# Optimization experiments

Hardware: AMD Instinct MI355X
Metric: run time of the kernel (lower is better)

## Reference

```python
import jax, jax.numpy as jnp
import numpy as np

KERNEL_SIZES = (3, 5, 7)
NUM_HEAD = 6
DIM = 192
K_SCALES = 3
HEADS_PER_SCALE = NUM_HEAD // K_SCALES  # 2
HEAD_DIM = DIM // NUM_HEAD              # 32
SCALE = HEAD_DIM ** -0.5


def _nbr_idx(L, K):
    # NATTEN non-causal, dilation=1: window centered on query, clamped at edges.
    start = jnp.clip(jnp.arange(L) - K // 2, 0, L - K)
    return start[:, None] + jnp.arange(K)  # [L, K]


def _na3d_branch(xi, K):
    # xi: [B, D, H, W, C] with C = 3 * HEADS_PER_SCALE * HEAD_DIM
    B, D, H, W, C = xi.shape
    qkv = xi.reshape(B, D, H, W, 3, HEADS_PER_SCALE, HEAD_DIM).transpose(4, 0, 5, 1, 2, 3, 6)
    q, k, v = qkv[0] * SCALE, qkv[1], qkv[2]  # each [B, h, D, H, W, hd]

    idd, idh, idw = _nbr_idx(D, K), _nbr_idx(H, K), _nbr_idx(W, K)

    def gather(t):
        t = jnp.take(t, idd, axis=2)  # [B,h,D,K,H,W,hd]
        t = jnp.take(t, idh, axis=4)  # [B,h,D,K,H,K,W,hd]
        t = jnp.take(t, idw, axis=6)  # [B,h,D,K,H,K,W,K,hd]
        return t

    kn = gather(k)
    vn = gather(v)
    # attention logits over the K^3 neighborhood per query
    attn = jnp.einsum('bndhwc,bndihjwkc->bndhwijk', q, kn)
    attn = jax.nn.softmax(attn.reshape(B, HEADS_PER_SCALE, D, H, W, K ** 3), axis=-1)
    attn = attn.reshape(B, HEADS_PER_SCALE, D, H, W, K, K, K)
    y = jnp.einsum('bndhwijk,bndihjwkc->bndhwc', attn, vn)
    # [B,h,D,H,W,hd] -> [B,D,H,W,h*hd]
    return y.transpose(0, 2, 3, 4, 1, 5).reshape(B, D, H, W, HEADS_PER_SCALE * HEAD_DIM)


def setup_inputs() -> dict:
    key = jax.random.key(0)
    k0, k1, k2 = jax.random.split(key, 3)
    x = jax.random.normal(k0, (1, 8, 24, 24, DIM), dtype=jnp.float32)
    W_qkv = jax.random.normal(k1, (DIM, 3 * DIM), dtype=jnp.float32) * 0.02
    b_qkv = jnp.zeros((3 * DIM,), dtype=jnp.float32)
    W_proj = jax.random.normal(k2, (DIM, DIM), dtype=jnp.float32) * 0.02
    b_proj = jnp.zeros((DIM,), dtype=jnp.float32)
    return {'x': x, 'W_qkv': W_qkv, 'b_qkv': b_qkv, 'W_proj': W_proj, 'b_proj': b_proj}


def reference(x, W_qkv, b_qkv, W_proj, b_proj):
    qkv = x @ W_qkv + b_qkv  # [B,D,H,W,3*DIM]
    # torch.split with channels [DIM, DIM, DIM]
    chunks = jnp.split(qkv, K_SCALES, axis=4)
    ys = [_na3d_branch(chunks[i], KERNEL_SIZES[i]) for i in range(K_SCALES)]
    y = jnp.concatenate(ys, axis=4)  # [B,D,H,W,DIM]
    return y @ W_proj + b_proj
```

## Files before the change

kernel.cpp:

```cpp
#include <hip/hip_runtime.h>

typedef unsigned short ushort_t;
typedef unsigned int uint_t;
typedef __attribute__((ext_vector_type(8))) short short8;
typedef __attribute__((ext_vector_type(4))) float f32x4;

constexpr int DD = 8, HH = 24, WW = 24;
constexpr int NQ = DD * HH * WW;
constexpr int CIN = 192;
constexpr int CQKV = 576;
constexpr int KP = 576;
constexpr float ATT_SCALE = 0.17677669529663687f;
constexpr int NROW = DD * HH;

__device__ __forceinline__ ushort_t bf16h(float x) {
    uint_t u = __float_as_uint(x);
    u += 0x7FFFu + ((u >> 16) & 1u);
    return (ushort_t)(u >> 16);
}
__device__ __forceinline__ float bf16f(ushort_t h) {
    return __uint_as_float(((uint_t)h) << 16);
}
__device__ __forceinline__ float2 unpack2(uint_t u) {
    return make_float2(__uint_as_float(u << 16),
                       __uint_as_float(u & 0xffff0000u));
}

constexpr int EB0 = 0;
constexpr int EB1 = NROW * 2 * WW * 2;
constexpr int EB2 = EB1 + NROW * 3 * WW * 2;
constexpr int ETOT = EB2 + NROW * 4 * WW * 2;

__global__ __launch_bounds__(256)
void convert_w_kernel(const float* __restrict__ Wq, const float* __restrict__ Wp,
                      ushort_t* __restrict__ Bq, ushort_t* __restrict__ Bp)
{
    __shared__ float T[32][36];
    int b = blockIdx.x;
    const float* W; ushort_t* Bb; int N;
    int kt, nt;
    if (b < 108) { W = Wq; Bb = Bq; N = CQKV; kt = b % 6; nt = b / 6; }
    else         { b -= 108; W = Wp; Bb = Bp; N = CIN; kt = b % 6; nt = b / 6; }
    const int k0 = kt * 32, n0 = nt * 32;
    const int tid = threadIdx.x;

    #pragma unroll
    for (int p = 0; p < 4; ++p) {
        int e = p * 256 + tid;
        int r = e >> 5, c = e & 31;
        T[c][r] = W[(long)(k0 + r) * N + n0 + c];
    }
    __syncthreads();
    const int n = tid >> 3;
    const int k4 = (tid & 7) * 4;
    float4 v = *(const float4*)(&T[n][k4]);
    ushort4 hv, lv;
    hv.x = bf16h(v.x); lv.x = bf16h(v.x - bf16f(hv.x));
    hv.y = bf16h(v.y); lv.y = bf16h(v.y - bf16f(hv.y));
    hv.z = bf16h(v.z); lv.z = bf16h(v.z - bf16f(hv.z));
    hv.w = bf16h(v.w); lv.w = bf16h(v.w - bf16f(hv.w));
    const int k = k0 + k4;
    const int g = k >> 6;
    const int kc = k & 63;
    ushort_t* row = Bb + (long)(n0 + n) * KP + g * 192 + kc;
    *(ushort4*)(row)       = hv;
    *(ushort4*)(row + 64)  = lv;
    *(ushort4*)(row + 128) = hv;
}

__global__ __launch_bounds__(256)
void gemm_mfma_kernel(const float* __restrict__ A, const ushort_t* __restrict__ Bb,
                      const float* __restrict__ bias, ushort_t* __restrict__ Cout, int N)
{
    __shared__ ushort_t As[64][72];
    __shared__ ushort_t Bs[64][72];
    __shared__ float Ct[64][68];

    const int tid = threadIdx.x;
    const int bm = blockIdx.x * 64;
    const int bn = blockIdx.y * 64;

    const int wv = tid >> 6;
    const int lane = tid & 63;
    const int lm = lane & 15;
    const int quad = lane >> 4;
    const int wr = (wv >> 1) * 32;
    const int wc = (wv & 1) * 32;

    const int ar = tid >> 4;
    const int ac4 = (tid & 15) * 4;
    const int br0 = tid >> 3;
    const int bc0 = (tid & 7) * 8;

    f32x4 acc[2][2] = {};

    #pragma unroll
    for (int g = 0; g < 3; ++g) {
        float4 av[4];
        ushort4 hv4[4];
        #pragma unroll
        for (int p = 0; p < 4; ++p)
            av[p] = *(const float4*)(A + (long)(bm + ar + p * 16) * CIN + g * 64 + ac4);

        #pragma unroll
        for (int ph = 0; ph < 3; ++ph) {
            const int kk = g * 192 + ph * 64;
            uint4 b0 = *(const uint4*)(Bb + (long)(bn + br0) * KP + kk + bc0);
            uint4 b1 = *(const uint4*)(Bb + (long)(bn + br0 + 32) * KP + kk + bc0);
            __syncthreads();
            if (ph == 0) {
                #pragma unroll
                for (int p = 0; p < 4; ++p) {
                    float4 v = av[p];
                    ushort4 hv;
                    hv.x = bf16h(v.x); hv.y = bf16h(v.y);
                    hv.z = bf16h(v.z); hv.w = bf16h(v.w);
                    hv4[p] = hv;
                    *(ushort4*)(&As[ar + p * 16][ac4]) = hv;
                }
            } else if (ph == 2) {
                #pragma unroll
                for (int p = 0; p < 4; ++p) {
                    float4 v = av[p];
                    ushort4 lv;
                    lv.x = bf16h(v.x - bf16f(hv4[p].x));
                    lv.y = bf16h(v.y - bf16f(hv4[p].y));
                    lv.z = bf16h(v.z - bf16f(hv4[p].z));
                    lv.w = bf16h(v.w - bf16f(hv4[p].w));
                    *(ushort4*)(&As[ar + p * 16][ac4]) = lv;
                }
            }
            *(uint4*)(&Bs[br0][bc0]) = b0;
            *(uint4*)(&Bs[br0 + 32][bc0]) = b1;
            __syncthreads();

            #pragma unroll
            for (int ks = 0; ks < 64; ks += 32) {
                short8 af0 = *(const short8*)(&As[wr + lm][ks + quad * 8]);
                short8 af1 = *(const short8*)(&As[wr + 16 + lm][ks + quad * 8]);
                short8 bf0 = *(const short8*)(&Bs[wc + lm][ks + quad * 8]);
                short8 bf1 = *(const short8*)(&Bs[wc + 16 + lm][ks + quad * 8]);
                acc[0][0] = __builtin_amdgcn_mfma_f32_16x16x32_bf16(af0, bf0, acc[0][0], 0, 0, 0);
                acc[0][1] = __builtin_amdgcn_mfma_f32_16x16x32_bf16(af0, bf1, acc[0][1], 0, 0, 0);
                acc[1][0] = __builtin_amdgcn_mfma_f32_16x16x32_bf16(af1, bf0, acc[1][0], 0, 0, 0);
                acc[1][1] = __builtin_amdgcn_mfma_f32_16x16x32_bf16(af1, bf1, acc[1][1], 0, 0, 0);
            }
        }
    }

    #pragma unroll
    for (int tc = 0; tc < 2; ++tc) {
        const float bv = bias[bn + wc + tc * 16 + lm];
        #pragma unroll
        for (int tr = 0; tr < 2; ++tr) {
            #pragma unroll
            for (int reg = 0; reg < 4; ++reg)
                Ct[wr + tr * 16 + quad * 4 + reg][wc + tc * 16 + lm] = acc[tr][tc][reg] + bv;
        }
    }
    __syncthreads();
    const int orow = tid >> 4;
    const int oc4 = (tid & 15) * 4;
    #pragma unroll
    for (int p = 0; p < 4; ++p) {
        const int r = orow + p * 16;
        float4 v = *(const float4*)(&Ct[r][oc4]);
        ushort4 hv;
        hv.x = bf16h(v.x); hv.y = bf16h(v.y); hv.z = bf16h(v.z); hv.w = bf16h(v.w);
        *(ushort4*)(Cout + (long)(bm + r) * N + bn + oc4) = hv;
    }
}

__global__ __launch_bounds__(256)
void gemm_proj_kernel(const float* __restrict__ accs, const float* __restrict__ stats,
                      const ushort_t* __restrict__ Bb, const float* __restrict__ bias,
                      float* __restrict__ Cout)
{
    __shared__ ushort_t As[64][72];
    __shared__ ushort_t Bs[64][72];
    __shared__ float Ct[64][68];

    const int tid = threadIdx.x;
    const int bm = blockIdx.x * 64;
    const int bn = blockIdx.y * 64;

    const int wv = tid >> 6;
    const int lane = tid & 63;
    const int lm = lane & 15;
    const int quad = lane >> 4;
    const int wr = (wv >> 1) * 32;
    const int wc = (wv & 1) * 32;

    const int ar = tid >> 4;
    const int ac4 = (tid & 15) * 4;
    const int a_hd = ac4 >> 5;
    const int a_cc = ac4 & 31;
    const int br0 = tid >> 3;
    const int bc0 = (tid & 7) * 8;

    f32x4 acc[2][2] = {};

    #pragma unroll
    for (int g = 0; g < 3; ++g) {
        const int CK = g + 2;
        const int eb = (g == 0) ? EB0 : (g == 1 ? EB1 : EB2);

        float4 av[4];
        ushort4 hv4[4];
        #pragma unroll
        for (int p = 0; p < 4; ++p) {
            const int q = bm + ar + p * 16;
            const int rr = q / WW;
            const int w = q - rr * WW;
            const int e0 = eb + (rr * CK) * (WW * 2) + w * 2 + a_hd;
            float S = 0.f;
            float4 a = make_float4(0.f, 0.f, 0.f, 0.f);
            #pragma unroll
            for (int c = 0; c < 4; ++c) {
                if (c < CK) {
                    const int e = e0 + c * (WW * 2);
                    S += stats[e];
                    const float4 t = *(const float4*)(accs + (long)e * 32 + a_cc);
                    a.x += t.x; a.y += t.y; a.z += t.z; a.w += t.w;
                }
            }
            const float rs = 1.0f / S;
            av[p] = make_float4(a.x * rs, a.y * rs, a.z * rs, a.w * rs);
        }

        #pragma unroll
        for (int ph = 0; ph < 3; ++ph) {
            const int kk = g * 192 + ph * 64;
            uint4 b0 = *(const uint4*)(Bb + (long)(bn + br0) * KP + kk + bc0);
            uint4 b1 = *(const uint4*)(Bb + (long)(bn + br0 + 32) * KP + kk + bc0);
            __syncthreads();
            if (ph == 0) {
                #pragma unroll
                for (int p = 0; p < 4; ++p) {
                    float4 v = av[p];
                    ushort4 hv;
                    hv.x = bf16h(v.x); hv.y = bf16h(v.y);
                    hv.z = bf16h(v.z); hv.w = bf16h(v.w);
                    hv4[p] = hv;
                    *(ushort4*)(&As[ar + p * 16][ac4]) = hv;
                }
            } else if (ph == 2) {
                #pragma unroll
                for (int p = 0; p < 4; ++p) {
                    float4 v = av[p];
                    ushort4 lv;
                    lv.x = bf16h(v.x - bf16f(hv4[p].x));
                    lv.y = bf16h(v.y - bf16f(hv4[p].y));
                    lv.z = bf16h(v.z - bf16f(hv4[p].z));
                    lv.w = bf16h(v.w - bf16f(hv4[p].w));
                    *(ushort4*)(&As[ar + p * 16][ac4]) = lv;
                }
            }
            *(uint4*)(&Bs[br0][bc0]) = b0;
            *(uint4*)(&Bs[br0 + 32][bc0]) = b1;
            __syncthreads();

            #pragma unroll
            for (int ks = 0; ks < 64; ks += 32) {
                short8 af0 = *(const short8*)(&As[wr + lm][ks + quad * 8]);
                short8 af1 = *(const short8*)(&As[wr + 16 + lm][ks + quad * 8]);
                short8 bf0 = *(const short8*)(&Bs[wc + lm][ks + quad * 8]);
                short8 bf1 = *(const short8*)(&Bs[wc + 16 + lm][ks + quad * 8]);
                acc[0][0] = __builtin_amdgcn_mfma_f32_16x16x32_bf16(af0, bf0, acc[0][0], 0, 0, 0);
                acc[0][1] = __builtin_amdgcn_mfma_f32_16x16x32_bf16(af0, bf1, acc[0][1], 0, 0, 0);
                acc[1][0] = __builtin_amdgcn_mfma_f32_16x16x32_bf16(af1, bf0, acc[1][0], 0, 0, 0);
                acc[1][1] = __builtin_amdgcn_mfma_f32_16x16x32_bf16(af1, bf1, acc[1][1], 0, 0, 0);
            }
        }
    }

    #pragma unroll
    for (int tc = 0; tc < 2; ++tc) {
        const float bv = bias[bn + wc + tc * 16 + lm];
        #pragma unroll
        for (int tr = 0; tr < 2; ++tr) {
            #pragma unroll
            for (int reg = 0; reg < 4; ++reg)
                Ct[wr + tr * 16 + quad * 4 + reg][wc + tc * 16 + lm] = acc[tr][tc][reg] + bv;
        }
    }
    __syncthreads();
    const int orow = tid >> 4;
    const int oc4 = (tid & 15) * 4;
    #pragma unroll
    for (int p = 0; p < 4; ++p) {
        const int r = orow + p * 16;
        float4 v = *(const float4*)(&Ct[r][oc4]);
        *(float4*)(Cout + (long)(bm + r) * CIN + bn + oc4) = v;
    }
}

constexpr int KROW = 72;
constexpr int RBUF = WW * KROW;

template<int K>
__device__ __forceinline__
void split_chunk(const ushort_t* __restrict__ qkv,
                 float* __restrict__ accs, float* __restrict__ stats,
                 int r, int c, int nchunks, int scale, int ebase,
                 int w, int hd, int d8, int tid,
                 ushort_t* __restrict__ ksh, ushort_t* __restrict__ vsh)
{
    const int i0 = 2 * c;
    const int ni = (K - i0) < 2 ? (K - i0) : 2;
    const int NT = ni * K;

    const int dq = r / HH, hq = r % HH;
    int sd = dq - K / 2; sd = sd < 0 ? 0 : (sd > DD - K ? DD - K : sd);
    int sh = hq - K / 2; sh = sh < 0 ? 0 : (sh > HH - K ? HH - K : sh);
    int sw = w  - K / 2; sw = sw < 0 ? 0 : (sw > WW - K ? WW - K : sw);

    const int q = (dq * HH + hq) * WW + w;

    uint4 qu = *(const uint4*)(qkv + (long)q * CQKV + scale * 192 + hd * 32 + d8 * 8);
    float2 qf[4] = {unpack2(qu.x), unpack2(qu.y), unpack2(qu.z), unpack2(qu.w)};
    #pragma unroll
    for (int t = 0; t < 4; ++t) {
        qf[t].x *= ATT_SCALE;
        qf[t].y *= ATT_SCALE;
    }

    const int lw = tid >> 3;
    const int c8 = (tid & 7) * 8;

    auto load_kv = [&](int buf, int t) {
        int i = i0 + t / K;
        int j = t - (t / K) * K;
        const ushort_t* p = qkv + (long)(((sd + i) * HH + (sh + j)) * WW + lw) * CQKV
                          + scale * 192 + c8;
        uint4 kk = *(const uint4*)(p + 64);
        uint4 vv = *(const uint4*)(p + 128);
        *(uint4*)(ksh + buf * RBUF + lw * KROW + c8) = kk;
        *(uint4*)(vsh + buf * RBUF + lw * KROW + c8) = vv;
    };

    float sum = 0.f;
    float2 acc[4] = {};
    const int choff = hd * 32 + d8 * 8;

    load_kv(0, 0);
    if (NT > 1) load_kv(1, 1);

    for (int t = 0; t < NT; ++t) {
        __syncthreads();
        if (t + 2 < NT) load_kv((t + 2) % 3, t + 2);

        const ushort_t* kb = ksh + (t % 3) * RBUF + choff;
        const ushort_t* vb = vsh + (t % 3) * RBUF + choff;
        #pragma unroll
        for (int n = 0; n < K; ++n) {
            uint4 ku = *(const uint4*)(kb + (sw + n) * KROW);
            float2 k0 = unpack2(ku.x), k1 = unpack2(ku.y),
                   k2 = unpack2(ku.z), k3 = unpack2(ku.w);
            float2 d;
            d.x  = qf[0].x * k0.x; d.y  = qf[0].y * k0.y;
            d.x += qf[1].x * k1.x; d.y += qf[1].y * k1.y;
            d.x += qf[2].x * k2.x; d.y += qf[2].y * k2.y;
            d.x += qf[3].x * k3.x; d.y += qf[3].y * k3.y;
            float p = d.x + d.y;
            p += __shfl_xor(p, 1);
            p += __shfl_xor(p, 2);
            float pr = __expf(p);
            sum += pr;
            uint4 vu = *(const uint4*)(vb + (sw + n) * KROW);
            float2 v0 = unpack2(vu.x), v1 = unpack2(vu.y),
                   v2 = unpack2(vu.z), v3 = unpack2(vu.w);
            acc[0].x += pr * v0.x; acc[0].y += pr * v0.y;
            acc[1].x += pr * v1.x; acc[1].y += pr * v1.y;
            acc[2].x += pr * v2.x; acc[2].y += pr * v2.y;
            acc[3].x += pr * v3.x; acc[3].y += pr * v3.y;
        }
    }

    const int e = ebase + ((r * nchunks + c) * WW + w) * 2 + hd;
    if (d8 == 0) stats[e] = sum;
    float* ap = accs + (long)e * 32 + d8 * 8;
    *(float4*)(ap)     = make_float4(acc[0].x, acc[0].y, acc[1].x, acc[1].y);
    *(float4*)(ap + 4) = make_float4(acc[2].x, acc[2].y, acc[3].x, acc[3].y);
}

__global__ __launch_bounds__(192)
void na3d_split_kernel(const ushort_t* __restrict__ qkv,
                       float* __restrict__ accs, float* __restrict__ stats)
{
    __shared__ alignas(16) ushort_t ksh[3 * RBUF];
    __shared__ alignas(16) ushort_t vsh[3 * RBUF];

    const int tid = threadIdx.x;
    const int w  = tid >> 3;
    const int hd = (tid >> 2) & 1;
    const int d8 = tid & 3;

    const int orig = blockIdx.x;
    int bid;
    if (orig < NROW * 4) {
        bid = (orig & 7) * (NROW * 4 / 8) + (orig >> 3);
    } else if (orig < NROW * 7) {
        const int t = orig - NROW * 4;
        bid = NROW * 4 + (t & 7) * (NROW * 3 / 8) + (t >> 3);
    } else {
        const int t = orig - NROW * 7;
        bid = NROW * 7 + (t & 7) * (NROW * 2 / 8) + (t >> 3);
    }

    if (bid < NROW * 4) {
        int r = bid >> 2, c = bid & 3;
        split_chunk<7>(qkv, accs, stats, r, c, 4, 2, EB2, w, hd, d8, tid, ksh, vsh);
    } else if (bid < NROW * 4 + NROW * 3) {
        int t = bid - NROW * 4;
        int r = t / 3, c = t - (t / 3) * 3;
        split_chunk<5>(qkv, accs, stats, r, c, 3, 1, EB1, w, hd, d8, tid, ksh, vsh);
    } else {
        int t = bid - NROW * 7;
        int r = t >> 1, c = t & 1;
        split_chunk<3>(qkv, accs, stats, r, c, 2, 0, EB0, w, hd, d8, tid, ksh, vsh);
    }
}

extern "C" void kernel_launch(void* const* d_in, const int* in_sizes, int n_in,
                              void* d_out, int out_size, void* d_ws, size_t ws_size,
                              hipStream_t stream)
{
    const float* x      = (const float*)d_in[0];
    const float* W_qkv  = (const float*)d_in[1];
    const float* b_qkv  = (const float*)d_in[2];
    const float* W_proj = (const float*)d_in[3];
    const float* b_proj = (const float*)d_in[4];
    float* out = (float*)d_out;

    float* accs    = (float*)d_ws;
    float* stats   = accs + (long)ETOT * 32;
    ushort_t* qkvb = (ushort_t*)(stats + ETOT);
    ushort_t* Wbq  = qkvb + (long)NQ * CQKV;
    ushort_t* Wbp  = Wbq + (long)CQKV * KP;

    convert_w_kernel<<<dim3(144), 256, 0, stream>>>(W_qkv, W_proj, Wbq, Wbp);

    gemm_mfma_kernel<<<dim3(NQ / 64, CQKV / 64), 256, 0, stream>>>(x, Wbq, b_qkv, qkvb, CQKV);

    na3d_split_kernel<<<dim3(NROW * (4 + 3 + 2)), 192, 0, stream>>>(qkvb, accs, stats);

    gemm_proj_kernel<<<dim3(NQ / 64, CIN / 64), 256, 0, stream>>>(accs, stats, Wbp, b_proj, out);
}
```

Before: 111.7 us.

## Register-prefetch GEMM and KV tiles, replace shuffles with DPP quad reductions

Both GEMM kernels now load the next B tile and the next A slab into registers one phase ahead, so global loads overlap the MFMA work of the current phase. The attention kernel holds the next K/V row in registers and writes it to shared memory after the compute loop, so global latency is hidden behind the math. The quad reductions use DPP moves instead of __shfl_xor, avoiding LDS-based cross-lane traffic. The cost is higher register pressure and reliance on exact DPP lane semantics.

Measured after the change: 110.4 us. Within noise of the previous version (-1.2%).

```diff
diff --git a/kernel.cpp b/kernel.cpp
--- a/kernel.cpp
+++ b/kernel.cpp
@@ -24,6 +24,12 @@
 __device__ __forceinline__ float2 unpack2(uint_t u) {
     return make_float2(__uint_as_float(u << 16),
                        __uint_as_float(u & 0xffff0000u));
+}
+__device__ __forceinline__ float quad_add_xor1(float x) {
+    return x + __int_as_float(__builtin_amdgcn_mov_dpp(__float_as_int(x), 0xB1, 0xF, 0xF, true));
+}
+__device__ __forceinline__ float quad_add_xor2(float x) {
+    return x + __int_as_float(__builtin_amdgcn_mov_dpp(__float_as_int(x), 0x4E, 0xF, 0xF, true));
 }
 
 constexpr int EB0 = 0;
@@ -94,19 +100,19 @@
 
     f32x4 acc[2][2] = {};
 
+    float4 av[4];
+    #pragma unroll
+    for (int p = 0; p < 4; ++p)
+        av[p] = *(const float4*)(A + (long)(bm + ar + p * 16) * CIN + ac4);
+    uint4 nb0 = *(const uint4*)(Bb + (long)(bn + br0) * KP + bc0);
+    uint4 nb1 = *(const uint4*)(Bb + (long)(bn + br0 + 32) * KP + bc0);
+
     #pragma unroll
     for (int g = 0; g < 3; ++g) {
-        float4 av[4];
         ushort4 hv4[4];
         #pragma unroll
-        for (int p = 0; p < 4; ++p)
-            av[p] = *(const float4*)(A + (long)(bm + ar + p * 16) * CIN + g * 64 + ac4);
-
-        #pragma unroll
         for (int ph = 0; ph < 3; ++ph) {
-            const int kk = g * 192 + ph * 64;
-            uint4 b0 = *(const uint4*)(Bb + (long)(bn + br0) * KP + kk + bc0);
-            uint4 b1 = *(const uint4*)(Bb + (long)(bn + br0 + 32) * KP + kk + bc0);
+            const uint4 b0 = nb0, b1 = nb1;
             __syncthreads();
             if (ph == 0) {
                 #pragma unroll
@@ -132,6 +138,17 @@
             }
             *(uint4*)(&Bs[br0][bc0]) = b0;
             *(uint4*)(&Bs[br0 + 32][bc0]) = b1;
+            const int nidx = g * 3 + ph + 1;
+            if (nidx < 9) {
+                const int nkk = (nidx / 3) * 192 + (nidx % 3) * 64;
+                nb0 = *(const uint4*)(Bb + (long)(bn + br0) * KP + nkk + bc0);
+                nb1 = *(const uint4*)(Bb + (long)(bn + br0 + 32) * KP + nkk + bc0);
+            }
+            if (ph == 2 && g < 2) {
+                #pragma unroll
+                for (int p = 0; p < 4; ++p)
+                    av[p] = *(const float4*)(A + (long)(bm + ar + p * 16) * CIN + (g + 1) * 64 + ac4);
+            }
             __syncthreads();
 
             #pragma unroll
@@ -200,13 +217,9 @@
 
     f32x4 acc[2][2] = {};
 
-    #pragma unroll
-    for (int g = 0; g < 3; ++g) {
-        const int CK = g + 2;
-        const int eb = (g == 0) ? EB0 : (g == 1 ? EB1 : EB2);
-
-        float4 av[4];
-        ushort4 hv4[4];
+    auto load_av = [&](int gg, float4* av) {
+        const int CK = gg + 2;
+        const int eb = (gg == 0) ? EB0 : (gg == 1 ? EB1 : EB2);
         #pragma unroll
         for (int p = 0; p < 4; ++p) {
             const int q = bm + ar + p * 16;
@@ -227,12 +240,19 @@
             const float rs = 1.0f / S;
             av[p] = make_float4(a.x * rs, a.y * rs, a.z * rs, a.w * rs);
         }
-
+    };
+
+    float4 av[4];
+    load_av(0, av);
+    uint4 nb0 = *(const uint4*)(Bb + (long)(bn + br0) * KP + bc0);
+    uint4 nb1 = *(const uint4*)(Bb + (long)(bn + br0 + 32) * KP + bc0);
+
+    #pragma unroll
+    for (int g = 0; g < 3; ++g) {
+        ushort4 hv4[4];
         #pragma unroll
         for (int ph = 0; ph < 3; ++ph) {
-            const int kk = g * 192 + ph * 64;
-            uint4 b0 = *(const uint4*)(Bb + (long)(bn + br0) * KP + kk + bc0);
-            uint4 b1 = *(const uint4*)(Bb + (long)(bn + br0 + 32) * KP + kk + bc0);
+            const uint4 b0 = nb0, b1 = nb1;
             __syncthreads();
             if (ph == 0) {
                 #pragma unroll
@@ -258,6 +278,14 @@
             }
             *(uint4*)(&Bs[br0][bc0]) = b0;
             *(uint4*)(&Bs[br0 + 32][bc0]) = b1;
+            const int nidx = g * 3 + ph + 1;
+            if (nidx < 9) {
+                const int nkk = (nidx / 3) * 192 + (nidx % 3) * 64;
+                nb0 = *(const uint4*)(Bb + (long)(bn + br0) * KP + nkk + bc0);
+                nb1 = *(const uint4*)(Bb + (long)(bn + br0 + 32) * KP + nkk + bc0);
+            }
+            if (ph == 2 && g < 2)
+                load_av(g + 1, av);
             __syncthreads();
 
             #pragma unroll
@@ -328,27 +356,38 @@
     const int lw = tid >> 3;
     const int c8 = (tid & 7) * 8;
 
-    auto load_kv = [&](int buf, int t) {
+    auto src_ptr = [&](int t) {
         int i = i0 + t / K;
         int j = t - (t / K) * K;
-        const ushort_t* p = qkv + (long)(((sd + i) * HH + (sh + j)) * WW + lw) * CQKV
-                          + scale * 192 + c8;
-        uint4 kk = *(const uint4*)(p + 64);
-        uint4 vv = *(const uint4*)(p + 128);
-        *(uint4*)(ksh + buf * RBUF + lw * KROW + c8) = kk;
-        *(uint4*)(vsh + buf * RBUF + lw * KROW + c8) = vv;
+        return qkv + (long)(((sd + i) * HH + (sh + j)) * WW + lw) * CQKV
+             + scale * 192 + c8;
     };
+
+    uint4 ck, cv;
+    {
+        const ushort_t* p0 = src_ptr(0);
+        uint4 k0 = *(const uint4*)(p0 + 64);
+        uint4 v0 = *(const uint4*)(p0 + 128);
+        const ushort_t* p1 = src_ptr(1);
+        ck = *(const uint4*)(p1 + 64);
+        cv = *(const uint4*)(p1 + 128);
+        *(uint4*)(ksh + lw * KROW + c8) = k0;
+        *(uint4*)(vsh + lw * KROW + c8) = v0;
+    }
 
     float sum = 0.f;
     float2 acc[4] = {};
     const int choff = hd * 32 + d8 * 8;
 
-    load_kv(0, 0);
-    if (NT > 1) load_kv(1, 1);
-
     for (int t = 0; t < NT; ++t) {
         __syncthreads();
-        if (t + 2 < NT) load_kv((t + 2) % 3, t + 2);
+        uint4 nk, nv;
+        const bool issue = (t + 2 < NT);
+        if (issue) {
+            const ushort_t* pn = src_ptr(t + 2);
+            nk = *(const uint4*)(pn + 64);
+            nv = *(const uint4*)(pn + 128);
+        }
 
         const ushort_t* kb = ksh + (t % 3) * RBUF + choff;
         const ushort_t* vb = vsh + (t % 3) * RBUF + choff;
@@ -363,8 +402,8 @@
             d.x += qf[2].x * k2.x; d.y += qf[2].y * k2.y;
             d.x += qf[3].x * k3.x; d.y += qf[3].y * k3.y;
             float p = d.x + d.y;
-            p += __shfl_xor(p, 1);
-            p += __shfl_xor(p, 2);
+            p = quad_add_xor1(p);
+            p = quad_add_xor2(p);
             float pr = __expf(p);
             sum += pr;
             uint4 vu = *(const uint4*)(vb + (sw + n) * KROW);
@@ -375,6 +414,12 @@
             acc[2].x += pr * v2.x; acc[2].y += pr * v2.y;
             acc[3].x += pr * v3.x; acc[3].y += pr * v3.y;
         }
+
+        if (t + 1 < NT) {
+            *(uint4*)(ksh + ((t + 1) % 3) * RBUF + lw * KROW + c8) = ck;
+            *(uint4*)(vsh + ((t + 1) % 3) * RBUF + lw * KROW + c8) = cv;
+        }
+        ck = nk; cv = nv;
     }
 
     const int e = ebase + ((r * nchunks + c) * WW + w) * 2 + hd;
```
